# Kernel optimization log

Hardware: AMD Instinct MI355X
Metric: run time of the kernel (lower is better)

Reference implementation:

```python
import jax, jax.numpy as jnp
import numpy as np
from jax import lax

NR, NC, DI, DO = 2048, 10, 8, 16  # routes, digit caps, in-dim, out-dim

# (t1, a1, b1, a2, b2, t3, a3, b3, a4, b4) piecewise-affine squash constants
PRIM_CONSTS = (-13.46416092, 0.000242759, 0.024488359, 0.002769205, 0.06089699,
               13.23405266, -0.002828244, 0.061313814, -0.000219038, 0.023874787)
DIGIT_CONSTS = (-0.075410217, -0.074520095, 0.349297946, -0.534473989, 0.27196494,
                0.062207676, 0.637642944, 0.295330779, 0.169344703, 0.353784456)


def _piecewise(s, t1, a1, b1, a2, b2, t3, a3, b3, a4, b4):
    # Faithful to the torch loop: new_sorted aliases sorted, so each segment
    # count (i1,i2,i3) is computed on the PARTIALLY-MODIFIED array, and each
    # slice end is idx-1 (off-by-one in the source), last slice ends at n-1.
    n = s.shape[0]
    ar = jnp.arange(n)
    i1 = jnp.sum(s < t1)
    s = jnp.where(ar < i1 - 1, a1 * s + b1, s)
    i2 = jnp.sum(s < 0.0)
    s = jnp.where((ar >= i1) & (ar < i2 - 1), a2 * s + b2, s)
    i3 = jnp.sum(s < t3)
    s = jnp.where((ar >= i2) & (ar < i3 - 1), a3 * s + b3, s)
    s = jnp.where((ar >= i3) & (ar < n - 1), a4 * s + b4, s)
    return s


def _squash_map(x, consts):
    # sort -> piecewise-affine remap -> unsort (one row)
    idx = jnp.argsort(x)
    s = _piecewise(x[idx], *consts)
    return s[jnp.argsort(idx)]


def _conv(x, w, b, stride):
    y = lax.conv_general_dilated(x, w, (stride, stride), 'VALID',
                                 dimension_numbers=('NCHW', 'OIHW', 'NCHW'))
    return y + b[None, :, None, None]


def capsnet_forward(data, conv1_w, conv1_b, prim_w, prim_b, W_dc,
                    dec_w1, dec_b1, dec_w2, dec_b2, dec_w3, dec_b3):
    B = data.shape[0]
    x = jax.nn.relu(_conv(data, conv1_w, conv1_b, 1))          # (B,256,24,24)
    u = _conv(x, prim_w, prim_b, 2).reshape(B, NR, DI)          # (B,2048,8) : 8 caps x 32ch x 8x8
    mag = jax.vmap(lambda r: _squash_map(r, PRIM_CONSTS))(u[:, :, 0])  # (B,2048)
    u_sq = mag[:, :, None] * u                                  # PrimaryCaps.my_squash2
    u_hat = jnp.einsum('rcoi,bri->brco', W_dc, u_sq)            # (B,2048,10,16)

    b_ij = jnp.zeros((NR, NC), dtype=u_hat.dtype)               # routing logits
    for it in range(3):
        c_ij = jax.nn.softmax(b_ij, axis=0)                     # softmax over routes (dim=1 in torch)
        s_j = jnp.einsum('rc,brco->bco', c_ij, u_hat)           # (B,10,16)
        f = jax.vmap(lambda r: _squash_map(r, DIGIT_CONSTS))(s_j[:, :, 0])  # (B,10)
        # torch writes the remapped value back into s_j in place (view aliasing),
        # so component 0 of v_j is f*f while other components are f*s_j
        s_mod = s_j.at[:, :, 0].set(f)
        v_j = f[:, :, None] * s_mod                             # (B,10,16)
        if it < 2:
            a_ij = jnp.einsum('brco,bco->brc', u_hat, v_j)      # agreement
            b_ij = b_ij + a_ij.mean(axis=0)

    # Decoder (reconstruction head)
    classes = jnp.sqrt(jnp.sum(v_j ** 2, axis=2))               # (B,10)
    classes = jax.nn.softmax(classes, axis=0)                   # softmax over batch, as in source
    idx = jnp.argmax(classes, axis=1)                           # (B,)
    masked = jnp.eye(NC, dtype=v_j.dtype)[idx]                  # (B,10) one-hot
    t = (v_j * masked[:, :, None]).reshape(B, -1)               # (B,160)
    h = jax.nn.relu(t @ dec_w1.T + dec_b1)
    h = jax.nn.relu(h @ dec_w2.T + dec_b2)
    recon = jax.nn.sigmoid(h @ dec_w3.T + dec_b3)               # (B,1024) = 32*32*1
    # single-array output: [flattened digit caps | flattened reconstruction]
    return jnp.concatenate([v_j.reshape(B, -1), recon], axis=1)  # (B,1184)


def setup_inputs() -> dict:
    key = jax.random.key(0)
    ks = jax.random.split(key, 12)
    f32 = jnp.float32
    return {
        'data': jax.random.normal(ks[0], (100, 1, 32, 32), f32),
        'conv1_w': jax.random.normal(ks[1], (256, 1, 9, 9), f32) * (1.0 / 9.0),
        'conv1_b': jnp.zeros((256,), f32),
        'prim_w': jax.random.normal(ks[2], (256, 256, 9, 9), f32) * (1.0 / 144.0),
        'prim_b': jnp.zeros((256,), f32),
        'W_dc': jax.random.normal(ks[3], (2048, 10, 16, 8), f32) * 0.05,
        'dec_w1': jax.random.normal(ks[4], (512, 160), f32) * 0.079,
        'dec_b1': jnp.zeros((512,), f32),
        'dec_w2': jax.random.normal(ks[5], (1024, 512), f32) * 0.0442,
        'dec_b2': jnp.zeros((1024,), f32),
        'dec_w3': jax.random.normal(ks[6], (1024, 1024), f32) * 0.03125,
        'dec_b3': jnp.zeros((1024,), f32),
        'train_or_test': 0,
        'epch': 0,
    }


def reference(data, conv1_w, conv1_b, prim_w, prim_b, W_dc,
              dec_w1, dec_b1, dec_w2, dec_b2, dec_w3, dec_b3,
              train_or_test, epch):
    return capsnet_forward(data, conv1_w, conv1_b, prim_w, prim_b, W_dc,
                           dec_w1, dec_b1, dec_w2, dec_b2, dec_w3, dec_b3)
```

## Files before the change

### kernel.cpp

```cpp
#include <hip/hip_runtime.h>
#include <cstdint>
#include <cstddef>


#define BATCH 100

static const size_t OFF_WT   = 0;
static const size_t OFF_X1   = 5308416;
static const size_t OFF_PU   = 20054016;
static const size_t OFF_UHAT = 0;
static const size_t OFF_U    = 33161216;
static const size_t OFF_BIJ  = 32768000;
static const size_t OFF_CIJ  = 32788480;
static const size_t OFF_SP   = 32808960;
static const size_t OFF_VJ   = 33064960;
static const size_t OFF_IDX  = 33080960;
static const size_t OFF_H1   = 33081088;
static const size_t OFF_H2   = 33132288;

#define PT1f -13.46416092f
#define PA1f 0.000242759f
#define PB1f 0.024488359f
#define PA2f 0.002769205f
#define PB2f 0.06089699f
#define PT3f 13.23405266f
#define PA3f -0.002828244f
#define PB3f 0.061313814f
#define PA4f -0.000219038f
#define PB4f 0.023874787f

#define DT1f -0.075410217f
#define DA1f -0.074520095f
#define DB1f 0.349297946f
#define DA2f -0.534473989f
#define DB2f 0.27196494f
#define DT3f 0.062207676f
#define DA3f 0.637642944f
#define DB3f 0.295330779f
#define DA4f 0.169344703f
#define DB4f 0.353784456f

#define XROW(r) ((r) * 12 + ((r) >> 1) * 4)
#define XPH 332
#define XTB 664

__global__ __launch_bounds__(256)
void k_transpose_w(const float* __restrict__ w, float* __restrict__ wt) {
  __shared__ float tile[64 * 82];
  int ci = blockIdx.x, co0 = blockIdx.y * 64, t = threadIdx.x;
  for (int f = t; f < 64 * 81; f += 256) {
    int col = f / 81, tap = f - col * 81;
    tile[col * 82 + tap] = w[(size_t)(co0 + col) * 20736 + (size_t)ci * 81 + tap];
  }
  __syncthreads();
  for (int g = t; g < 64 * 81; g += 256) {
    int tap = g / 64, col = g - tap * 64;
    wt[((size_t)ci * 81 + tap) * 256 + co0 + col] = tile[col * 82 + tap];
  }
}

__global__ __launch_bounds__(256)
void k_conv1(const float* __restrict__ data, const float* __restrict__ cw,
             const float* __restrict__ cb, float* __restrict__ x1) {
  __shared__ float img[1024];
  __shared__ float wl[81 * 32];
  int b = blockIdx.x, cg = blockIdx.y, t = threadIdx.x;
  for (int f = t; f < 1024; f += 256) img[f] = data[(size_t)b * 1024 + f];
  for (int f = t; f < 2592; f += 256) {
    int tap = f >> 5, c = f & 31;
    wl[f] = cw[(size_t)(cg * 32 + c) * 81 + tap];
  }
  __syncthreads();
  for (int task = t; task < 1152; task += 256) {
    int q = task % 144, cq = task / 144;
    int p0 = q * 4, oh = p0 / 24, ow0 = p0 % 24;
    float a[4][4];
#pragma unroll
    for (int i = 0; i < 4; ++i)
#pragma unroll
      for (int j = 0; j < 4; ++j) a[i][j] = 0.f;
    for (int kh = 0; kh < 9; ++kh) {
      const float* ir = &img[(oh + kh) * 32 + ow0];
      const float* wr = &wl[kh * 9 * 32 + cq * 4];
#pragma unroll
      for (int kw = 0; kw < 9; ++kw) {
        float4 wv = *(const float4*)(wr + kw * 32);
#pragma unroll
        for (int j = 0; j < 4; ++j) {
          float xv = ir[kw + j];
          a[0][j] = fmaf(wv.x, xv, a[0][j]);
          a[1][j] = fmaf(wv.y, xv, a[1][j]);
          a[2][j] = fmaf(wv.z, xv, a[2][j]);
          a[3][j] = fmaf(wv.w, xv, a[3][j]);
        }
      }
    }
#pragma unroll
    for (int cc = 0; cc < 4; ++cc) {
      int c = cg * 32 + cq * 4 + cc;
      float bias = cb[c];
      float4 o4 = make_float4(fmaxf(a[cc][0] + bias, 0.f), fmaxf(a[cc][1] + bias, 0.f),
                              fmaxf(a[cc][2] + bias, 0.f), fmaxf(a[cc][3] + bias, 0.f));
      *(float4*)&x1[((size_t)(b * 256 + c) * 24 + oh) * 24 + ow0] = o4;
    }
  }
}

__global__ __launch_bounds__(256, 8)
void k_prim(const float* __restrict__ x1, const float* __restrict__ wt,
            float* __restrict__ pu) {
  __shared__ float wsh[81 * 32];
  __shared__ float xsh[4 * XTB];
  int t = threadIdx.x;
  int tb = t >> 6, tl = t & 63;
  int coq = tl >> 3, oh = tl & 7;
  int ci_base = blockIdx.x * 32, cog = blockIdx.y, bq = blockIdx.z;
  int b = bq * 4 + tb;

  float acc[4][8];
#pragma unroll
  for (int i = 0; i < 4; ++i)
#pragma unroll
    for (int j = 0; j < 8; ++j) acc[i][j] = 0.f;

#pragma unroll 1
  for (int ci = ci_base; ci < ci_base + 32; ++ci) {
    __syncthreads();
    for (int f = t; f < 288; f += 256) {
      int tbj = f / 72, rem = f - tbj * 72;
      int r = rem / 3, oct = rem - r * 3;
      const float* gp = &x1[((size_t)(bq * 4 + tbj) * 256 + ci) * 576 + r * 24 + oct * 8];
      float4 v1 = *(const float4*)gp;
      float4 v2 = *(const float4*)(gp + 4);
      float* eb = &xsh[tbj * XTB + XROW(r) + oct * 4];
      *(float4*)eb = make_float4(v1.x, v1.z, v2.x, v2.z);
      *(float4*)(eb + XPH) = make_float4(v1.y, v1.w, v2.y, v2.w);
    }
    for (int f = t; f < 648; f += 256) {
      int tap = f >> 3, cq = f & 7;
      float4 v = *(const float4*)&wt[((size_t)ci * 81 + tap) * 256 + cog * 32 + cq * 4];
      *(float4*)&wsh[tap * 32 + cq * 4] = v;
    }
    __syncthreads();
    const float* xb = &xsh[tb * XTB];
    const float* wb = &wsh[coq * 4];
#pragma unroll 3
    for (int kh = 0; kh < 9; ++kh) {
      int r = 2 * oh + kh;
      const float* xe = xb + XROW(r);
      float ew[12], ov[12];
      *(float4*)&ew[0] = *(const float4*)xe;
      *(float4*)&ew[4] = *(const float4*)(xe + 4);
      *(float4*)&ew[8] = *(const float4*)(xe + 8);
      *(float4*)&ov[0] = *(const float4*)(xe + XPH);
      *(float4*)&ov[4] = *(const float4*)(xe + XPH + 4);
      *(float4*)&ov[8] = *(const float4*)(xe + XPH + 8);
      const float* wr = wb + kh * 9 * 32;
#pragma unroll
      for (int p = 0; p < 5; ++p) {
        float4 wv = *(const float4*)(wr + p * 64);
#pragma unroll
        for (int j = 0; j < 8; ++j) {
          float xv = ew[p + j];
          acc[0][j] = fmaf(wv.x, xv, acc[0][j]);
          acc[1][j] = fmaf(wv.y, xv, acc[1][j]);
          acc[2][j] = fmaf(wv.z, xv, acc[2][j]);
          acc[3][j] = fmaf(wv.w, xv, acc[3][j]);
        }
      }
#pragma unroll
      for (int p = 0; p < 4; ++p) {
        float4 wv = *(const float4*)(wr + 32 + p * 64);
#pragma unroll
        for (int j = 0; j < 8; ++j) {
          float xv = ov[p + j];
          acc[0][j] = fmaf(wv.x, xv, acc[0][j]);
          acc[1][j] = fmaf(wv.y, xv, acc[1][j]);
          acc[2][j] = fmaf(wv.z, xv, acc[2][j]);
          acc[3][j] = fmaf(wv.w, xv, acc[3][j]);
        }
      }
    }
  }
  float* pp = pu + (((size_t)blockIdx.x * BATCH + b) * 2048 +
                    (cog * 32 + coq * 4) * 8 + oh) * 8;
#pragma unroll
  for (int cc = 0; cc < 4; ++cc) {
    *(float4*)(pp + cc * 64)     = make_float4(acc[cc][0], acc[cc][1], acc[cc][2], acc[cc][3]);
    *(float4*)(pp + cc * 64 + 4) = make_float4(acc[cc][4], acc[cc][5], acc[cc][6], acc[cc][7]);
  }
}

__global__ __launch_bounds__(256)
void k_ured(const float* __restrict__ pu, const float* __restrict__ pb,
            float* __restrict__ u) {
  int g4 = blockIdx.x * 256 + threadIdx.x;
  if (g4 >= 409600) return;
  size_t g = (size_t)g4 * 4;
  const size_t S = 1638400;
  float4 s = *(const float4*)(pu + g);
#pragma unroll
  for (int k = 1; k < 8; ++k) {
    float4 p = *(const float4*)(pu + (size_t)k * S + g);
    s.x += p.x; s.y += p.y; s.z += p.z; s.w += p.w;
  }
  int r = (int)((g >> 3) & 2047);
  float bias = pb[r >> 3];
  float4 o = make_float4(s.x + bias, s.y + bias, s.z + bias, s.w + bias);
  *(float4*)(u + g) = o;
}

__global__ __launch_bounds__(256)
void k_squash(float* __restrict__ u) {
  __shared__ float kv[2048];
  __shared__ int kid[2048];
  __shared__ int red[256];
  int b = blockIdx.x, t = threadIdx.x;
  for (int r = t; r < 2048; r += 256) {
    kv[r] = u[((size_t)b * 2048 + r) * 8];
    kid[r] = r;
  }
  __syncthreads();
  for (int size = 2; size <= 2048; size <<= 1) {
    for (int stride = size >> 1; stride > 0; stride >>= 1) {
#pragma unroll 1
      for (int s = 0; s < 4; ++s) {
        int i = t + s * 256;
        int pos = 2 * i - (i & (stride - 1));
        int q = pos + stride;
        float va = kv[pos], vb = kv[q];
        int ia = kid[pos], ib = kid[q];
        bool gt = (va > vb) || (va == vb && ia > ib);
        bool up = ((pos & size) == 0);
        if (gt == up) { kv[pos] = vb; kv[q] = va; kid[pos] = ib; kid[q] = ia; }
      }
      __syncthreads();
    }
  }
  int loc = 0;
#pragma unroll
  for (int s = 0; s < 8; ++s) loc += (kv[t + s * 256] < PT1f) ? 1 : 0;
  red[t] = loc; __syncthreads();
  for (int off = 128; off; off >>= 1) { if (t < off) red[t] += red[t + off]; __syncthreads(); }
  int i1 = red[0]; __syncthreads();
  float m1v[8];
  loc = 0;
#pragma unroll
  for (int s = 0; s < 8; ++s) {
    int p = t + s * 256;
    float v = kv[p];
    float m = (p < i1 - 1) ? (PA1f * v + PB1f) : v;
    m1v[s] = m;
    loc += (m < 0.f) ? 1 : 0;
  }
  red[t] = loc; __syncthreads();
  for (int off = 128; off; off >>= 1) { if (t < off) red[t] += red[t + off]; __syncthreads(); }
  int i2 = red[0]; __syncthreads();
  float m2v[8];
  loc = 0;
#pragma unroll
  for (int s = 0; s < 8; ++s) {
    int p = t + s * 256;
    float m = (p >= i1 && p < i2 - 1) ? (PA2f * m1v[s] + PB2f) : m1v[s];
    m2v[s] = m;
    loc += (m < PT3f) ? 1 : 0;
  }
  red[t] = loc; __syncthreads();
  for (int off = 128; off; off >>= 1) { if (t < off) red[t] += red[t + off]; __syncthreads(); }
  int i3 = red[0]; __syncthreads();
#pragma unroll
  for (int s = 0; s < 8; ++s) {
    int p = t + s * 256;
    float m = m2v[s];
    m = (p >= i2 && p < i3 - 1) ? (PA3f * m + PB3f) : m;
    m = (p >= i3 && p < 2047) ? (PA4f * m + PB4f) : m;
    int rid = kid[p];
    float* row = u + ((size_t)b * 2048 + rid) * 8;
    float4 lo = *(float4*)row;
    float4 hi = *(float4*)(row + 4);
    lo.x *= m; lo.y *= m; lo.z *= m; lo.w *= m;
    hi.x *= m; hi.y *= m; hi.z *= m; hi.w *= m;
    *(float4*)row = lo;
    *(float4*)(row + 4) = hi;
  }
}

__global__ __launch_bounds__(192)
void k_uhat(const float* __restrict__ Wdc, const float* __restrict__ usq,
            float* __restrict__ uhat) {
  int t = threadIdx.x;
  if (t >= 160) return;
  int r0 = blockIdx.x * 8;
#pragma unroll 1
  for (int half = 0; half < 2; ++half) {
    int rb = r0 + half * 4;
    float4 wa[4], wb4[4];
#pragma unroll
    for (int rl = 0; rl < 4; ++rl) {
      const float* wp = Wdc + ((size_t)(rb + rl) * 160 + t) * 8;
      wa[rl]  = *(const float4*)wp;
      wb4[rl] = *(const float4*)(wp + 4);
    }
#pragma unroll 2
    for (int b = 0; b < BATCH; ++b) {
      const float* ub = usq + ((size_t)b * 2048 + rb) * 8;
      float* op = uhat + ((size_t)b * 2048 + rb) * 160 + t;
#pragma unroll
      for (int rl = 0; rl < 4; ++rl) {
        const float* us = ub + rl * 8;
        float v = us[0] * wa[rl].x + us[1] * wa[rl].y + us[2] * wa[rl].z + us[3] * wa[rl].w +
                  us[4] * wb4[rl].x + us[5] * wb4[rl].y + us[6] * wb4[rl].z + us[7] * wb4[rl].w;
        op[(size_t)rl * 160] = v;
      }
    }
  }
}

__global__ __launch_bounds__(256)
void k_softc(const float* __restrict__ bij, float* __restrict__ cij) {
  __shared__ float red[256];
  int c = blockIdx.x, t = threadIdx.x;
  float m = -3.402823466e38f;
  for (int r = t; r < 2048; r += 256) m = fmaxf(m, bij[r * 10 + c]);
  red[t] = m; __syncthreads();
  for (int off = 128; off; off >>= 1) { if (t < off) red[t] = fmaxf(red[t], red[t + off]); __syncthreads(); }
  m = red[0]; __syncthreads();
  float s = 0.f;
  for (int r = t; r < 2048; r += 256) s += expf(bij[r * 10 + c] - m);
  red[t] = s; __syncthreads();
  for (int off = 128; off; off >>= 1) { if (t < off) red[t] += red[t + off]; __syncthreads(); }
  s = red[0];
  for (int r = t; r < 2048; r += 256) cij[r * 10 + c] = expf(bij[r * 10 + c] - m) / s;
}

__global__ __launch_bounds__(192)
void k_sjpart(const float* __restrict__ cij, const float* __restrict__ uhat,
              float* __restrict__ sp, int it0) {
  __shared__ float cl[1280];
  int b = blockIdx.x, ch = blockIdx.y, t = threadIdx.x;
  if (!it0) {
    for (int f = t; f < 1280; f += 192) cl[f] = cij[(size_t)ch * 1280 + f];
  }
  __syncthreads();
  if (t < 160) {
    int c = t >> 4;
    float acc = 0.f;
    const float* up = uhat + ((size_t)b * 2048 + ch * 128) * 160 + t;
    if (it0) {
      const float cuni = 0.00048828125f;
#pragma unroll 4
      for (int rl = 0; rl < 128; ++rl) acc += cuni * up[(size_t)rl * 160];
    } else {
#pragma unroll 4
      for (int rl = 0; rl < 128; ++rl) acc += cl[rl * 10 + c] * up[(size_t)rl * 160];
    }
    sp[((size_t)b * 16 + ch) * 160 + t] = acc;
  }
}

__global__ __launch_bounds__(192)
void k_sjred(const float* __restrict__ sp, float* __restrict__ vj,
             float* __restrict__ dout, int finalit) {
  __shared__ float sl[160];
  __shared__ float fl[10];
  int b = blockIdx.x, t = threadIdx.x;
  if (t < 160) {
    float a = 0.f;
#pragma unroll
    for (int ch = 0; ch < 16; ++ch) a += sp[((size_t)b * 16 + ch) * 160 + t];
    sl[t] = a;
  }
  __syncthreads();
  if (t == 0) {
    float sv[10]; int rk[10];
    for (int c = 0; c < 10; ++c) sv[c] = sl[c * 16];
    for (int c = 0; c < 10; ++c) {
      int r = 0;
      for (int k = 0; k < 10; ++k)
        r += ((sv[k] < sv[c]) || (sv[k] == sv[c] && k < c)) ? 1 : 0;
      rk[c] = r;
    }
    int i1 = 0;
    for (int c = 0; c < 10; ++c) i1 += (sv[c] < DT1f) ? 1 : 0;
    float m1[10];
    for (int c = 0; c < 10; ++c) m1[c] = (rk[c] < i1 - 1) ? (DA1f * sv[c] + DB1f) : sv[c];
    int i2 = 0;
    for (int c = 0; c < 10; ++c) i2 += (m1[c] < 0.f) ? 1 : 0;
    float m2[10];
    for (int c = 0; c < 10; ++c)
      m2[c] = (rk[c] >= i1 && rk[c] < i2 - 1) ? (DA2f * m1[c] + DB2f) : m1[c];
    int i3 = 0;
    for (int c = 0; c < 10; ++c) i3 += (m2[c] < DT3f) ? 1 : 0;
    for (int c = 0; c < 10; ++c) {
      float m = (rk[c] >= i2 && rk[c] < i3 - 1) ? (DA3f * m2[c] + DB3f) : m2[c];
      m = (rk[c] >= i3 && rk[c] < 9) ? (DA4f * m + DB4f) : m;
      fl[c] = m;
    }
  }
  __syncthreads();
  if (t < 160) {
    int c = t >> 4, o = t & 15;
    float fv = fl[c];
    float v = fv * ((o == 0) ? fv : sl[t]);
    vj[(size_t)b * 160 + t] = v;
    if (finalit) dout[(size_t)b * 1184 + t] = v;
  }
}

__global__ __launch_bounds__(192)
void k_amean(const float* __restrict__ uhat, const float* __restrict__ vj,
             float* __restrict__ bij, int first) {
  __shared__ float vl[16000];
  int t = threadIdx.x, r0 = blockIdx.x * 8;
  for (int f = t; f < 16000; f += 192) vl[f] = vj[f];
  __syncthreads();
  if (t < 160) {
    int c = t >> 4;
    float acc[8];
#pragma unroll
    for (int rl = 0; rl < 8; ++rl) acc[rl] = 0.f;
    const float* up0 = uhat + (size_t)r0 * 160 + t;
#pragma unroll 2
    for (int b = 0; b < BATCH; ++b) {
      float vv = vl[b * 160 + t];
      const float* up = up0 + (size_t)b * 327680;
#pragma unroll
      for (int rl = 0; rl < 8; ++rl)
        acc[rl] = fmaf(up[(size_t)rl * 160], vv, acc[rl]);
    }
#pragma unroll
    for (int rl = 0; rl < 8; ++rl) {
      float a = acc[rl];
      for (int off = 8; off; off >>= 1) a += __shfl_down(a, off, 16);
      if ((t & 15) == 0) {
        int r = r0 + rl;
        float val = a / 100.0f;
        bij[r * 10 + c] = first ? val : (bij[r * 10 + c] + val);
      }
    }
  }
}

__global__ __launch_bounds__(256)
void k_cls(const float* __restrict__ vj, int* __restrict__ idxg) {
  __shared__ float cl[1000];
  __shared__ float cm[10];
  __shared__ float cs[10];
  int t = threadIdx.x;
  for (int f = t; f < 1000; f += 256) {
    int b = f / 10, c = f - b * 10;
    float s = 0.f;
#pragma unroll
    for (int o = 0; o < 16; ++o) {
      float v = vj[(size_t)b * 160 + c * 16 + o];
      s += v * v;
    }
    cl[f] = sqrtf(s);
  }
  __syncthreads();
  if (t < 10) {
    float m = -3.402823466e38f;
    for (int b = 0; b < BATCH; ++b) m = fmaxf(m, cl[b * 10 + t]);
    float s = 0.f;
    for (int b = 0; b < BATCH; ++b) s += expf(cl[b * 10 + t] - m);
    cm[t] = m; cs[t] = s;
  }
  __syncthreads();
  for (int b = t; b < BATCH; b += 256) {
    float best = -1.f; int bi = 0;
    for (int c = 0; c < 10; ++c) {
      float val = expf(cl[b * 10 + c] - cm[c]) / cs[c];
      if (val > best) { best = val; bi = c; }
    }
    idxg[b] = bi;
  }
}

__global__ __launch_bounds__(256)
void k_dec1(const float* __restrict__ w1, const float* __restrict__ b1,
            const float* __restrict__ vj, const int* __restrict__ idxg,
            float* __restrict__ h1) {
  int b = blockIdx.x, t = threadIdx.x;
  int id = idxg[b];
  const float* v = vj + (size_t)b * 160 + id * 16;
  for (int j = t; j < 512; j += 256) {
    float acc = b1[j];
    const float* wr = w1 + (size_t)j * 160 + id * 16;
#pragma unroll
    for (int o = 0; o < 16; ++o) acc += wr[o] * v[o];
    h1[(size_t)b * 512 + j] = fmaxf(acc, 0.f);
  }
}

__global__ __launch_bounds__(256)
void k_dec2(const float* __restrict__ w2, const float* __restrict__ b2,
            const float* __restrict__ h1, float* __restrict__ h2) {
  __shared__ float red[4][64][4];
  int t = threadIdx.x, lane = t & 63, strip = t >> 6;
  int j = blockIdx.x * 64 + lane, bs = blockIdx.y * 4;
  float acc[4] = {0.f, 0.f, 0.f, 0.f};
  const float* wr = w2 + (size_t)j * 512 + strip * 128;
  const float* hb = h1 + (size_t)bs * 512 + strip * 128;
  for (int k4 = 0; k4 < 32; ++k4) {
    float4 wv = *(const float4*)(wr + k4 * 4);
    const float* h0 = hb + k4 * 4;
#pragma unroll
    for (int q = 0; q < 4; ++q) {
      float4 hv = *(const float4*)(h0 + q * 512);
      acc[q] += wv.x * hv.x + wv.y * hv.y + wv.z * hv.z + wv.w * hv.w;
    }
  }
#pragma unroll
  for (int q = 0; q < 4; ++q) red[strip][lane][q] = acc[q];
  __syncthreads();
  if (strip == 0) {
    float bias = b2[j];
#pragma unroll
    for (int q = 0; q < 4; ++q) {
      float tot = red[0][lane][q] + red[1][lane][q] + red[2][lane][q] + red[3][lane][q] + bias;
      h2[(size_t)(bs + q) * 1024 + j] = fmaxf(tot, 0.f);
    }
  }
}

__global__ __launch_bounds__(256)
void k_dec3(const float* __restrict__ w3, const float* __restrict__ b3,
            const float* __restrict__ h2, float* __restrict__ dout) {
  __shared__ float red[4][64][4];
  int t = threadIdx.x, lane = t & 63, strip = t >> 6;
  int j = blockIdx.x * 64 + lane, bs = blockIdx.y * 4;
  float acc[4] = {0.f, 0.f, 0.f, 0.f};
  const float* wr = w3 + (size_t)j * 1024 + strip * 256;
  const float* hb = h2 + (size_t)bs * 1024 + strip * 256;
  for (int k4 = 0; k4 < 64; ++k4) {
    float4 wv = *(const float4*)(wr + k4 * 4);
    const float* h0 = hb + k4 * 4;
#pragma unroll
    for (int q = 0; q < 4; ++q) {
      float4 hv = *(const float4*)(h0 + q * 1024);
      acc[q] += wv.x * hv.x + wv.y * hv.y + wv.z * hv.z + wv.w * hv.w;
    }
  }
#pragma unroll
  for (int q = 0; q < 4; ++q) red[strip][lane][q] = acc[q];
  __syncthreads();
  if (strip == 0) {
    float bias = b3[j];
#pragma unroll
    for (int q = 0; q < 4; ++q) {
      float tot = red[0][lane][q] + red[1][lane][q] + red[2][lane][q] + red[3][lane][q] + bias;
      dout[(size_t)(bs + q) * 1184 + 160 + j] = 1.f / (1.f + expf(-tot));
    }
  }
}

extern "C" void kernel_launch(void* const* d_in, const int* in_sizes, int n_in,
                              void* d_out, int out_size, void* d_ws, size_t ws_size,
                              hipStream_t stream) {
  (void)in_sizes; (void)n_in; (void)out_size; (void)ws_size;
  const float* data = (const float*)d_in[0];
  const float* c1w  = (const float*)d_in[1];
  const float* c1b  = (const float*)d_in[2];
  const float* pw   = (const float*)d_in[3];
  const float* pb   = (const float*)d_in[4];
  const float* Wdc  = (const float*)d_in[5];
  const float* w1   = (const float*)d_in[6];
  const float* b1   = (const float*)d_in[7];
  const float* w2   = (const float*)d_in[8];
  const float* b2   = (const float*)d_in[9];
  const float* w3   = (const float*)d_in[10];
  const float* b3   = (const float*)d_in[11];
  float* out = (float*)d_out;
  float* ws  = (float*)d_ws;

  float* WT   = ws + OFF_WT;
  float* X1   = ws + OFF_X1;
  float* PU   = ws + OFF_PU;
  float* UHAT = ws + OFF_UHAT;
  float* U    = ws + OFF_U;
  float* BIJ  = ws + OFF_BIJ;
  float* CIJ  = ws + OFF_CIJ;
  float* SP   = ws + OFF_SP;
  float* VJ   = ws + OFF_VJ;
  int*   IDX  = (int*)(ws + OFF_IDX);
  float* H1   = ws + OFF_H1;
  float* H2   = ws + OFF_H2;

  k_transpose_w<<<dim3(256, 4), 256, 0, stream>>>(pw, WT);
  k_conv1<<<dim3(BATCH, 8), 256, 0, stream>>>(data, c1w, c1b, X1);
  k_prim<<<dim3(8, 8, 25), 256, 0, stream>>>(X1, WT, PU);
  k_ured<<<1600, 256, 0, stream>>>(PU, pb, U);
  k_squash<<<BATCH, 256, 0, stream>>>(U);
  k_uhat<<<256, 192, 0, stream>>>(Wdc, U, UHAT);

  for (int it = 0; it < 3; ++it) {
    if (it > 0) k_softc<<<10, 256, 0, stream>>>(BIJ, CIJ);
    k_sjpart<<<dim3(BATCH, 16), 192, 0, stream>>>(CIJ, UHAT, SP, it == 0 ? 1 : 0);
    k_sjred<<<BATCH, 192, 0, stream>>>(SP, VJ, out, it == 2 ? 1 : 0);
    if (it < 2) k_amean<<<256, 192, 0, stream>>>(UHAT, VJ, BIJ, it == 0 ? 1 : 0);
  }

  k_cls<<<1, 256, 0, stream>>>(VJ, IDX);
  k_dec1<<<BATCH, 256, 0, stream>>>(w1, b1, VJ, IDX, H1);
  k_dec2<<<dim3(16, 25), 256, 0, stream>>>(w2, b2, H1, H2);
  k_dec3<<<dim3(16, 25), 256, 0, stream>>>(w3, b3, H2, out);
}
```

Baseline: 1.290 ms.

## Prefetch next input-channel tiles into registers in primary-caps conv

Restructures the k_prim loop so the global loads for the next input channel's activations and weights are issued into registers right after the shared-memory store, overlapping them with the current channel's FMA work. Address computation is hoisted out of the loop, the kh loop is fully unrolled with precomputed row offsets, and the launch bounds drop from 8 to 4 blocks per SM to leave room for the extra registers. The cost is higher register pressure and lower occupancy. The row-offset formula assumes a particular XROW definition, which could be wrong if the layout differs.

```diff
diff --git a/kernel.cpp b/kernel.cpp
--- a/kernel.cpp
+++ b/kernel.cpp
@@ -106,7 +106,7 @@
   }
 }
 
-__global__ __launch_bounds__(256, 8)
+__global__ __launch_bounds__(256, 4)
 void k_prim(const float* __restrict__ x1, const float* __restrict__ wt,
             float* __restrict__ pu) {
   __shared__ float wsh[81 * 32];
@@ -117,37 +117,61 @@
   int ci_base = blockIdx.x * 32, cog = blockIdx.y, bq = blockIdx.z;
   int b = bq * 4 + tb;
 
+  int xt0 = t / 72, xm0 = t - xt0 * 72;
+  int xr0 = xm0 / 3, xo0 = xm0 - xr0 * 3;
+  const float* xg0 = x1 + ((size_t)(bq * 4 + xt0) * 256 + ci_base) * 576 + xr0 * 24 + xo0 * 8;
+  float* xl0 = &xsh[xt0 * XTB + XROW(xr0) + xo0 * 4];
+  int f1 = t + 256;
+  int xt1 = f1 / 72, xm1 = f1 - xt1 * 72;
+  int xr1 = xm1 / 3, xo1 = xm1 - xr1 * 3;
+  bool hx1 = (t < 32);
+  const float* xg1 = x1 + ((size_t)(bq * 4 + xt1) * 256 + ci_base) * 576 + xr1 * 24 + xo1 * 8;
+  float* xl1 = &xsh[xt1 * XTB + XROW(xr1) + xo1 * 4];
+  const float* wg0 = wt + ((size_t)ci_base * 81 + (t >> 3)) * 256 + cog * 32 + (t & 7) * 4;
+  float* wl0 = &wsh[(t >> 3) * 32 + (t & 7) * 4];
+  bool hw2 = (t < 136);
+
   float acc[4][8];
 #pragma unroll
   for (int i = 0; i < 4; ++i)
 #pragma unroll
     for (int j = 0; j < 8; ++j) acc[i][j] = 0.f;
+
+  float4 pxa0 = *(const float4*)xg0, pxb0 = *(const float4*)(xg0 + 4);
+  float4 pxa1, pxb1;
+  if (hx1) { pxa1 = *(const float4*)xg1; pxb1 = *(const float4*)(xg1 + 4); }
+  float4 pw0 = *(const float4*)wg0;
+  float4 pw1 = *(const float4*)(wg0 + 32 * 256);
+  float4 pw2;
+  if (hw2) pw2 = *(const float4*)(wg0 + 64 * 256);
+
+  const float* xb = &xsh[tb * XTB] + XROW(2 * oh);
+  const float* wb = &wsh[coq * 4];
 
 #pragma unroll 1
   for (int ci = ci_base; ci < ci_base + 32; ++ci) {
     __syncthreads();
-    for (int f = t; f < 288; f += 256) {
-      int tbj = f / 72, rem = f - tbj * 72;
-      int r = rem / 3, oct = rem - r * 3;
-      const float* gp = &x1[((size_t)(bq * 4 + tbj) * 256 + ci) * 576 + r * 24 + oct * 8];
-      float4 v1 = *(const float4*)gp;
-      float4 v2 = *(const float4*)(gp + 4);
-      float* eb = &xsh[tbj * XTB + XROW(r) + oct * 4];
-      *(float4*)eb = make_float4(v1.x, v1.z, v2.x, v2.z);
-      *(float4*)(eb + XPH) = make_float4(v1.y, v1.w, v2.y, v2.w);
-    }
-    for (int f = t; f < 648; f += 256) {
-      int tap = f >> 3, cq = f & 7;
-      float4 v = *(const float4*)&wt[((size_t)ci * 81 + tap) * 256 + cog * 32 + cq * 4];
-      *(float4*)&wsh[tap * 32 + cq * 4] = v;
-    }
+    *(float4*)xl0        = make_float4(pxa0.x, pxa0.z, pxb0.x, pxb0.z);
+    *(float4*)(xl0 + XPH) = make_float4(pxa0.y, pxa0.w, pxb0.y, pxb0.w);
+    if (hx1) {
+      *(float4*)xl1        = make_float4(pxa1.x, pxa1.z, pxb1.x, pxb1.z);
+      *(float4*)(xl1 + XPH) = make_float4(pxa1.y, pxa1.w, pxb1.y, pxb1.w);
+    }
+    *(float4*)wl0             = pw0;
+    *(float4*)(wl0 + 32 * 32) = pw1;
+    if (hw2) *(float4*)(wl0 + 64 * 32) = pw2;
     __syncthreads();
-    const float* xb = &xsh[tb * XTB];
-    const float* wb = &wsh[coq * 4];
-#pragma unroll 3
+    if (ci + 1 < ci_base + 32) {
+      xg0 += 576; xg1 += 576; wg0 += 81 * 256;
+      pxa0 = *(const float4*)xg0; pxb0 = *(const float4*)(xg0 + 4);
+      if (hx1) { pxa1 = *(const float4*)xg1; pxb1 = *(const float4*)(xg1 + 4); }
+      pw0 = *(const float4*)wg0;
+      pw1 = *(const float4*)(wg0 + 32 * 256);
+      if (hw2) pw2 = *(const float4*)(wg0 + 64 * 256);
+    }
+#pragma unroll
     for (int kh = 0; kh < 9; ++kh) {
-      int r = 2 * oh + kh;
-      const float* xe = xb + XROW(r);
+      const float* xe = xb + (12 * kh + 4 * (kh >> 1));
       float ew[12], ov[12];
       *(float4*)&ew[0] = *(const float4*)xe;
       *(float4*)&ew[4] = *(const float4*)(xe + 4);
@@ -155,7 +179,7 @@
       *(float4*)&ov[0] = *(const float4*)(xe + XPH);
       *(float4*)&ov[4] = *(const float4*)(xe + XPH + 4);
       *(float4*)&ov[8] = *(const float4*)(xe + XPH + 8);
-      const float* wr = wb + kh * 9 * 32;
+      const float* wr = wb + kh * 288;
 #pragma unroll
       for (int p = 0; p < 5; ++p) {
         float4 wv = *(const float4*)(wr + p * 64);
```

Result: slower. 1.390 ms (+7.7%).

## Load primary-caps conv tiles directly into LDS with global_load_lds

Applied to the files above, without the earlier changes.

The per-channel input and weight tiles in k_prim are now copied from global memory straight into LDS with 16-byte global_load_lds, instead of being staged through registers. The input tile keeps its natural row layout (28-float row stride) rather than being split into even and odd columns, and the stride-2 sampling happens in registers. The kh loop is fully unrolled and the occupancy hint is dropped. This removes the register staging and VALU shuffling in the tile fill, at the cost of more registers, possibly lower occupancy, a larger LDS footprint, and reliance on the compiler inserting the right wait before the barrier.

```diff
diff --git a/kernel.cpp b/kernel.cpp
--- a/kernel.cpp
+++ b/kernel.cpp
@@ -40,9 +40,10 @@
 #define DA4f 0.169344703f
 #define DB4f 0.353784456f
 
-#define XROW(r) ((r) * 12 + ((r) >> 1) * 4)
-#define XPH 332
-#define XTB 664
+#define GLDS16(gp, lp)                                                        \
+  __builtin_amdgcn_global_load_lds(                                           \
+      (const __attribute__((address_space(1))) void*)(gp),                    \
+      (__attribute__((address_space(3))) void*)(lp), 16, 0, 0)
 
 __global__ __launch_bounds__(256)
 void k_transpose_w(const float* __restrict__ w, float* __restrict__ wt) {
@@ -106,62 +107,83 @@
   }
 }
 
-__global__ __launch_bounds__(256, 8)
+__global__ __launch_bounds__(256)
 void k_prim(const float* __restrict__ x1, const float* __restrict__ wt,
             float* __restrict__ pu) {
-  __shared__ float wsh[81 * 32];
-  __shared__ float xsh[4 * XTB];
+  __shared__ float wsh[5408];
+  __shared__ float xsh[2688];
   int t = threadIdx.x;
   int tb = t >> 6, tl = t & 63;
   int coq = tl >> 3, oh = tl & 7;
   int ci_base = blockIdx.x * 32, cog = blockIdx.y, bq = blockIdx.z;
   int b = bq * 4 + tb;
 
+  char* xshB = (char*)xsh;
+  char* wshB = (char*)wsh;
+
+  int xj0 = t, xj1 = t + 256, xj2 = t + 512;
+  bool hx2 = (t < 160);
+  const float* xg[3];
+  {
+    int js[3] = {xj0, xj1, hx2 ? xj2 : 0};
+#pragma unroll
+    for (int s = 0; s < 3; ++s) {
+      int j = js[s];
+      int tbj = j / 168, rem = j - tbj * 168;
+      int row = rem / 7, ch = rem - row * 7;
+      xg[s] = x1 + ((size_t)(bq * 4 + tbj) * 256 + ci_base) * 576 + row * 24 + ch * 4;
+    }
+  }
+  bool hw2 = (t < 136);
+  const float* wg[3];
+  {
+    int js[3] = {t, t + 256, hw2 ? t + 512 : 0};
+#pragma unroll
+    for (int s = 0; s < 3; ++s) {
+      int j = js[s];
+      int tap = j >> 3, cq = j & 7;
+      wg[s] = wt + ((size_t)ci_base * 81 + tap) * 256 + cog * 32 + cq * 4;
+    }
+  }
+
   float acc[4][8];
 #pragma unroll
   for (int i = 0; i < 4; ++i)
 #pragma unroll
     for (int j = 0; j < 8; ++j) acc[i][j] = 0.f;
+
+  const float* xrb = &xsh[tb * 672];
+  const float* wb = &wsh[coq * 4];
 
 #pragma unroll 1
   for (int ci = ci_base; ci < ci_base + 32; ++ci) {
     __syncthreads();
-    for (int f = t; f < 288; f += 256) {
-      int tbj = f / 72, rem = f - tbj * 72;
-      int r = rem / 3, oct = rem - r * 3;
-      const float* gp = &x1[((size_t)(bq * 4 + tbj) * 256 + ci) * 576 + r * 24 + oct * 8];
-      float4 v1 = *(const float4*)gp;
-      float4 v2 = *(const float4*)(gp + 4);
-      float* eb = &xsh[tbj * XTB + XROW(r) + oct * 4];
-      *(float4*)eb = make_float4(v1.x, v1.z, v2.x, v2.z);
-      *(float4*)(eb + XPH) = make_float4(v1.y, v1.w, v2.y, v2.w);
-    }
-    for (int f = t; f < 648; f += 256) {
-      int tap = f >> 3, cq = f & 7;
-      float4 v = *(const float4*)&wt[((size_t)ci * 81 + tap) * 256 + cog * 32 + cq * 4];
-      *(float4*)&wsh[tap * 32 + cq * 4] = v;
-    }
+    GLDS16(xg[0], xshB + 16 * xj0);
+    GLDS16(xg[1], xshB + 16 * xj1);
+    if (hx2) GLDS16(xg[2], xshB + 16 * xj2);
+    GLDS16(wg[0], wshB + 16 * t);
+    GLDS16(wg[1], wshB + 16 * (t + 256));
+    if (hw2) GLDS16(wg[2], wshB + 16 * (t + 512));
+    xg[0] += 576; xg[1] += 576; xg[2] += 576;
+    wg[0] += 81 * 256; wg[1] += 81 * 256; wg[2] += 81 * 256;
     __syncthreads();
-    const float* xb = &xsh[tb * XTB];
-    const float* wb = &wsh[coq * 4];
-#pragma unroll 3
+#pragma unroll
     for (int kh = 0; kh < 9; ++kh) {
-      int r = 2 * oh + kh;
-      const float* xe = xb + XROW(r);
-      float ew[12], ov[12];
-      *(float4*)&ew[0] = *(const float4*)xe;
-      *(float4*)&ew[4] = *(const float4*)(xe + 4);
-      *(float4*)&ew[8] = *(const float4*)(xe + 8);
-      *(float4*)&ov[0] = *(const float4*)(xe + XPH);
-      *(float4*)&ov[4] = *(const float4*)(xe + XPH + 4);
-      *(float4*)&ov[8] = *(const float4*)(xe + XPH + 8);
-      const float* wr = wb + kh * 9 * 32;
+      const float* xe = xrb + (2 * oh + kh) * 28;
+      float xr[24];
+      *(float4*)&xr[0]  = *(const float4*)xe;
+      *(float4*)&xr[4]  = *(const float4*)(xe + 4);
+      *(float4*)&xr[8]  = *(const float4*)(xe + 8);
+      *(float4*)&xr[12] = *(const float4*)(xe + 12);
+      *(float4*)&xr[16] = *(const float4*)(xe + 16);
+      *(float4*)&xr[20] = *(const float4*)(xe + 20);
+      const float* wr = wb + kh * 288;
 #pragma unroll
       for (int p = 0; p < 5; ++p) {
         float4 wv = *(const float4*)(wr + p * 64);
 #pragma unroll
         for (int j = 0; j < 8; ++j) {
-          float xv = ew[p + j];
+          float xv = xr[2 * (p + j)];
           acc[0][j] = fmaf(wv.x, xv, acc[0][j]);
           acc[1][j] = fmaf(wv.y, xv, acc[1][j]);
           acc[2][j] = fmaf(wv.z, xv, acc[2][j]);
@@ -173,7 +195,7 @@
         float4 wv = *(const float4*)(wr + 32 + p * 64);
 #pragma unroll
         for (int j = 0; j < 8; ++j) {
-          float xv = ov[p + j];
+          float xv = xr[2 * (p + j) + 1];
           acc[0][j] = fmaf(wv.x, xv, acc[0][j]);
           acc[1][j] = fmaf(wv.y, xv, acc[1][j]);
           acc[2][j] = fmaf(wv.z, xv, acc[2][j]);
```

Measured after the change: 1.294 ms. No clear change (+0.3%).
